# Kernel tuning notes

Hardware: AMD Instinct MI355X
Metric: run time of the kernel (lower is better)

## Reference

```python
import jax, jax.numpy as jnp
import numpy as np

N = 8192       # n_nodes
D = 256        # conf.unify['dim']
GAMMA = 3.0    # conf.unify['gamma']
ALPHA = 0.5    # conf.unify['alpha']
EPS = 1e-6


def setup_inputs() -> dict:
    key = jax.random.key(0)
    k1, k2, k3, k4 = jax.random.split(key, 4)
    z = jax.random.normal(k1, (N, D), dtype=jnp.float32)
    # kaiming-uniform-ish scale for W
    W = jax.random.normal(k2, (D, D), dtype=jnp.float32) * (1.0 / np.sqrt(D))
    beta = jax.random.uniform(k3, (N, 1), dtype=jnp.float32)      # beta_vector, init ~0.5
    Q = jax.random.uniform(k4, (N, N), dtype=jnp.float32)          # nonnegative prior (dense stand-in for sparse Q)
    return {"z": z, "W": W, "beta": beta, "Q": Q}


def reference(z, W, beta, Q):
    # init-time: Q row-normalized (normalize(Q, style='row'))
    Qn = Q / jnp.sum(Q, axis=1, keepdims=True)            # [N, N]

    # 1. similarity: sim = (z @ W) @ z.T
    sim = (z @ W) @ z.T                                    # [N, N]

    # 2. sparsify: relu(sim - beta), relu + eps, power 1/(gamma-1)
    adj = jax.nn.relu(sim - beta)                          # beta [N,1] broadcasts over columns
    adj = jax.nn.relu(adj) + EPS                           # relu_with_eps
    adj = adj ** (1.0 / (GAMMA - 1.0))                     # gamma power-law sparsify

    # 3. fuse Q: (1-alpha)*adj + alpha*(adj*Q), then /N
    adj = (1.0 - ALPHA) * adj + ALPHA * (adj * Qn)
    adj = adj / N

    # 4. row-normalize
    adj = adj / jnp.sum(adj, axis=-1, keepdims=True)
    return adj
```

## Files before the change

kernel.cpp:

```cpp
#include <hip/hip_runtime.h>
#include <hip/hip_bf16.h>
#include <math.h>

#define N 8192
#define D 256
#define EPSF 1e-6f

typedef __attribute__((ext_vector_type(8))) short short8v;
typedef __attribute__((ext_vector_type(4))) float f32x4;
typedef __attribute__((ext_vector_type(4))) unsigned short u16x4;

__device__ __forceinline__ unsigned short f2bf(float x) {
    __hip_bfloat16 h = __float2bfloat16(x);
    return *(unsigned short*)&h;
}
__device__ __forceinline__ float bf2f(unsigned short u) {
    __hip_bfloat16 h = *(__hip_bfloat16*)&u;
    return __bfloat162float(h);
}
__device__ __forceinline__ float bfu2f(unsigned short u) {
    unsigned int x = ((unsigned int)u) << 16;
    float f;
    __builtin_memcpy(&f, &x, 4);
    return f;
}
__device__ __forceinline__ f32x4 ntload4(const float* p) {
    return __builtin_nontemporal_load((const f32x4*)p);
}
__device__ __forceinline__ void ntstore4(float* p, f32x4 v) {
    __builtin_nontemporal_store(v, (f32x4*)p);
}

#define GLOAD_LDS16(gp, lp)                                                                  \
    __builtin_amdgcn_global_load_lds((const __attribute__((address_space(1))) unsigned int*)(gp), \
                                     (__attribute__((address_space(3))) unsigned int*)(lp), 16, 0, 0)

__global__ __launch_bounds__(256) void split_kernel(const float* __restrict__ x,
                                                    unsigned short* __restrict__ hi,
                                                    unsigned short* __restrict__ lo) {
    int i = (blockIdx.x * 256 + threadIdx.x) * 4;
    float4 v = *(const float4*)&x[i];
    ushort4 h, l;
    float a;
    a = v.x; h.x = f2bf(a); l.x = f2bf(a - bf2f(h.x));
    a = v.y; h.y = f2bf(a); l.y = f2bf(a - bf2f(h.y));
    a = v.z; h.z = f2bf(a); l.z = f2bf(a - bf2f(h.z));
    a = v.w; h.w = f2bf(a); l.w = f2bf(a - bf2f(h.w));
    *(ushort4*)&hi[i] = h;
    *(ushort4*)&lo[i] = l;
}

__global__ __launch_bounds__(256) void zw_kernel(const float* __restrict__ z,
                                                 const float* __restrict__ W,
                                                 unsigned short* __restrict__ Ah,
                                                 unsigned short* __restrict__ Al) {
    __shared__ float zs[32 * D];
    int rowBase = blockIdx.x * 32;
    const float4* zg = (const float4*)(z + (size_t)rowBase * D);
    float4* zs4 = (float4*)zs;
    for (int i = threadIdx.x; i < 32 * D / 4; i += 256) zs4[i] = zg[i];
    __syncthreads();

    float acc[32];
#pragma unroll
    for (int r = 0; r < 32; ++r) acc[r] = 0.f;
    int col = threadIdx.x;
    for (int kb = 0; kb < D; kb += 4) {
        float w0 = W[(size_t)(kb + 0) * D + col];
        float w1 = W[(size_t)(kb + 1) * D + col];
        float w2 = W[(size_t)(kb + 2) * D + col];
        float w3 = W[(size_t)(kb + 3) * D + col];
#pragma unroll
        for (int r = 0; r < 32; ++r) {
            float4 zv = *(const float4*)&zs[r * D + kb];
            acc[r] = fmaf(zv.x, w0, acc[r]);
            acc[r] = fmaf(zv.y, w1, acc[r]);
            acc[r] = fmaf(zv.z, w2, acc[r]);
            acc[r] = fmaf(zv.w, w3, acc[r]);
        }
    }
#pragma unroll
    for (int r = 0; r < 32; ++r) {
        float a = acc[r];
        unsigned short h = f2bf(a);
        unsigned short l = f2bf(a - bf2f(h));
        Ah[(size_t)(rowBase + r) * D + col] = h;
        Al[(size_t)(rowBase + r) * D + col] = l;
    }
}

__device__ __forceinline__ void tile_map(int bid, int& rowBase, int& colBase) {
    int xcd = bid & 7;
    int idx = bid >> 3;
    int bx = idx >> 3;
    int by = xcd * 8 + (idx & 7);
    rowBase = by * 128;
    colBase = bx * 128;
}

template <bool BF16S>
__global__ __launch_bounds__(256, 4) void gemm_s_kernel(
    const unsigned short* __restrict__ Ah, const unsigned short* __restrict__ Al,
    const unsigned short* __restrict__ Bh, const unsigned short* __restrict__ Bl,
    const float* __restrict__ beta, unsigned short* __restrict__ sbf,
    float* __restrict__ sf32) {
    __shared__ unsigned short lds[4][128][32];

    int rowBase, colBase;
    tile_map(blockIdx.x, rowBase, colBase);

    int t = threadIdx.x;
    int lane = t & 63;
    int w = t >> 6;
    int wr = w >> 1, wc = w & 1;
    int fr = lane & 15;
    int fg = lane >> 4;

    const unsigned short* tsrc = (w == 0) ? Ah : (w == 1) ? Al : (w == 2) ? Bh : Bl;
    int tRB = (w < 2) ? rowBase : colBase;
    int slot_src = (lane & 3) ^ ((lane >> 3) & 3);
    const unsigned short* gt = tsrc + (size_t)(tRB + (lane >> 2)) * D + slot_src * 8;

    f32x4 acc[4][4];
#pragma unroll
    for (int m = 0; m < 4; ++m)
#pragma unroll
        for (int n = 0; n < 4; ++n) acc[m][n] = (f32x4){0.f, 0.f, 0.f, 0.f};

    for (int kt = 0; kt < D; kt += 32) {
        __syncthreads();
#pragma unroll
        for (int j = 0; j < 8; ++j) {
            GLOAD_LDS16(gt + kt + j * 16 * D, &lds[w][j * 16][0]);
        }
        __syncthreads();

        short8v bhf[4], blf[4];
#pragma unroll
        for (int n = 0; n < 4; ++n) {
            int row = wc * 64 + n * 16 + fr;
            int sl = fg ^ ((row >> 1) & 3);
            bhf[n] = *(const short8v*)&lds[2][row][sl * 8];
            blf[n] = *(const short8v*)&lds[3][row][sl * 8];
        }
#pragma unroll
        for (int m = 0; m < 4; ++m) {
            int row = wr * 64 + m * 16 + fr;
            int sl = fg ^ ((row >> 1) & 3);
            short8v ahf = *(const short8v*)&lds[0][row][sl * 8];
            short8v alf = *(const short8v*)&lds[1][row][sl * 8];
#pragma unroll
            for (int n = 0; n < 4; ++n) {
                acc[m][n] = __builtin_amdgcn_mfma_f32_16x16x32_bf16(ahf, bhf[n], acc[m][n], 0, 0, 0);
                acc[m][n] = __builtin_amdgcn_mfma_f32_16x16x32_bf16(ahf, blf[n], acc[m][n], 0, 0, 0);
                acc[m][n] = __builtin_amdgcn_mfma_f32_16x16x32_bf16(alf, bhf[n], acc[m][n], 0, 0, 0);
            }
        }
    }

    __syncthreads();
    float* scratch = (float*)lds + w * (16 * 68);

#pragma unroll
    for (int m = 0; m < 4; ++m) {
#pragma unroll
        for (int n = 0; n < 4; ++n)
#pragma unroll
            for (int reg = 0; reg < 4; ++reg)
                scratch[(fg * 4 + reg) * 68 + n * 16 + fr] = acc[m][n][reg];

#pragma unroll
        for (int sub = 0; sub < 4; ++sub) {
            int rloc = sub * 4 + fg;
            int i = rowBase + wr * 64 + m * 16 + rloc;
            int col = colBase + wc * 64 + fr * 4;
            float4 sv = *(const float4*)&scratch[rloc * 68 + fr * 4];
            float bi = beta[i];
            float s0 = sqrtf(fmaxf(sv.x - bi, 0.f) + EPSF);
            float s1 = sqrtf(fmaxf(sv.y - bi, 0.f) + EPSF);
            float s2 = sqrtf(fmaxf(sv.z - bi, 0.f) + EPSF);
            float s3 = sqrtf(fmaxf(sv.w - bi, 0.f) + EPSF);
            if constexpr (BF16S) {
                u16x4 o = {f2bf(s0), f2bf(s1), f2bf(s2), f2bf(s3)};
                __builtin_nontemporal_store(o, (u16x4*)(sbf + (size_t)i * N + col));
            } else {
                f32x4 o = {s0, s1, s2, s3};
                ntstore4(sf32 + (size_t)i * N + col, o);
            }
        }
        __syncthreads();
    }
}

template <bool BF16S>
__global__ __launch_bounds__(512) void rownorm_kernel(float* __restrict__ out,
                                                      const float* __restrict__ Q,
                                                      const unsigned short* __restrict__ sbf) {
    __shared__ short8v sb[N / 8];
    __shared__ short8v qb[N / 8];
    __shared__ float red[24];

    int row = blockIdx.x;
    int t = threadIdx.x;
    const float* qrow = Q + (size_t)row * N;

    float ps = 0.f, pq = 0.f, qs = 0.f;
    for (int k = t; k < N / 8; k += 512) {
        float s[8];
        short8v spack;
        if constexpr (BF16S) {
            spack = __builtin_nontemporal_load((const short8v*)(sbf + (size_t)row * N + k * 8));
#pragma unroll
            for (int j = 0; j < 8; ++j) s[j] = bfu2f((unsigned short)spack[j]);
        } else {
            f32x4 a = ntload4(out + (size_t)row * N + k * 8);
            f32x4 b = ntload4(out + (size_t)row * N + k * 8 + 4);
            s[0] = a.x; s[1] = a.y; s[2] = a.z; s[3] = a.w;
            s[4] = b.x; s[5] = b.y; s[6] = b.z; s[7] = b.w;
#pragma unroll
            for (int j = 0; j < 8; ++j) spack[j] = (short)f2bf(s[j]);
        }
        sb[k] = spack;
        f32x4 q0 = ntload4(qrow + k * 8);
        f32x4 q1 = ntload4(qrow + k * 8 + 4);
        float q[8] = {q0.x, q0.y, q0.z, q0.w, q1.x, q1.y, q1.z, q1.w};
        short8v qpack;
#pragma unroll
        for (int j = 0; j < 8; ++j) qpack[j] = (short)f2bf(q[j]);
        qb[k] = qpack;
#pragma unroll
        for (int j = 0; j < 8; ++j) {
            ps += s[j];
            pq += s[j] * q[j];
            qs += q[j];
        }
    }
#pragma unroll
    for (int off = 1; off < 64; off <<= 1) {
        ps += __shfl_xor(ps, off, 64);
        pq += __shfl_xor(pq, off, 64);
        qs += __shfl_xor(qs, off, 64);
    }
    if ((t & 63) == 0) {
        int wv = t >> 6;
        red[wv * 3 + 0] = ps;
        red[wv * 3 + 1] = pq;
        red[wv * 3 + 2] = qs;
    }
    __syncthreads();
    float tps = 0.f, tpq = 0.f, tqs = 0.f;
#pragma unroll
    for (int i = 0; i < 8; ++i) {
        tps += red[i * 3 + 0];
        tpq += red[i * 3 + 1];
        tqs += red[i * 3 + 2];
    }
    float sh = 0.5f / tqs;
    float wv = 1.0f / (0.5f * tps + sh * tpq);

    float* orow = out + (size_t)row * N;
    for (int k = t; k < N / 8; k += 512) {
        short8v sp = sb[k];
        short8v qp = qb[k];
        f32x4 o0, o1;
#pragma unroll
        for (int j = 0; j < 4; ++j)
            o0[j] = bfu2f((unsigned short)sp[j]) * fmaf(bfu2f((unsigned short)qp[j]), sh, 0.5f) * wv;
#pragma unroll
        for (int j = 0; j < 4; ++j)
            o1[j] = bfu2f((unsigned short)sp[j + 4]) * fmaf(bfu2f((unsigned short)qp[j + 4]), sh, 0.5f) * wv;
        ntstore4(orow + k * 8, o0);
        ntstore4(orow + k * 8 + 4, o1);
    }
}

extern "C" void kernel_launch(void* const* d_in, const int* in_sizes, int n_in,
                              void* d_out, int out_size, void* d_ws, size_t ws_size,
                              hipStream_t stream) {
    const float* z = (const float*)d_in[0];
    const float* W = (const float*)d_in[1];
    const float* beta = (const float*)d_in[2];
    const float* Q = (const float*)d_in[3];
    float* out = (float*)d_out;

    unsigned short* Ah = (unsigned short*)d_ws;
    unsigned short* Al = Ah + (size_t)N * D;
    unsigned short* Bh = Al + (size_t)N * D;
    unsigned short* Bl = Bh + (size_t)N * D;
    unsigned short* sbf = Bl + (size_t)N * D;

    size_t need = 4 * (size_t)N * D * sizeof(unsigned short) + (size_t)N * N * sizeof(unsigned short);
    bool bf16s = (ws_size >= need);

    split_kernel<<<(N * D / 4) / 256, 256, 0, stream>>>(z, Bh, Bl);
    zw_kernel<<<N / 32, 256, 0, stream>>>(z, W, Ah, Al);
    if (bf16s) {
        gemm_s_kernel<true><<<4096, 256, 0, stream>>>(Ah, Al, Bh, Bl, beta, sbf, nullptr);
        rownorm_kernel<true><<<N, 512, 0, stream>>>(out, Q, sbf);
    } else {
        gemm_s_kernel<false><<<4096, 256, 0, stream>>>(Ah, Al, Bh, Bl, beta, nullptr, out);
        rownorm_kernel<false><<<N, 512, 0, stream>>>(out, Q, nullptr);
    }
}
```

Measured before the change: 303.7 us.

## Enlarge similarity GEMM tile to 256x256 with double-buffered LDS prefetch

The similarity GEMM moves from 128x128 tiles with 256 threads to 256x256 tiles with 512 threads, so each block reuses its A and B operands across four times as much output. The K loop now double-buffers LDS: the next K slice is staged while the current one feeds the MFMAs, which cuts one barrier per iteration. MFMA sections are wrapped in s_setprio. The trade-off is 128KB of LDS per block, which limits the kernel to one block per CU and leaves fewer blocks to hide latency. Correctness also depends on the async global-to-LDS loads having completed before the single per-iteration barrier.

```diff
diff --git a/kernel.cpp b/kernel.cpp
--- a/kernel.cpp
+++ b/kernel.cpp
@@ -89,80 +89,88 @@
     }
 }
 
-__device__ __forceinline__ void tile_map(int bid, int& rowBase, int& colBase) {
-    int xcd = bid & 7;
-    int idx = bid >> 3;
-    int bx = idx >> 3;
-    int by = xcd * 8 + (idx & 7);
-    rowBase = by * 128;
-    colBase = bx * 128;
-}
-
 template <bool BF16S>
-__global__ __launch_bounds__(256, 4) void gemm_s_kernel(
+__global__ __launch_bounds__(512, 2) void gemm_s_kernel(
     const unsigned short* __restrict__ Ah, const unsigned short* __restrict__ Al,
     const unsigned short* __restrict__ Bh, const unsigned short* __restrict__ Bl,
     const float* __restrict__ beta, unsigned short* __restrict__ sbf,
     float* __restrict__ sf32) {
-    __shared__ unsigned short lds[4][128][32];
-
-    int rowBase, colBase;
-    tile_map(blockIdx.x, rowBase, colBase);
+    __shared__ unsigned short lds[2][4][256][32];
+
+    int bid = blockIdx.x;
+    int xcd = bid & 7;
+    int idx = bid >> 3;
+    int rowIn = idx & 3;
+    int bx = idx >> 2;
+    int by = xcd * 4 + rowIn;
+    int rowBase = by * 256;
+    int colBase = bx * 256;
 
     int t = threadIdx.x;
     int lane = t & 63;
     int w = t >> 6;
-    int wr = w >> 1, wc = w & 1;
+    int wr = w >> 2, wc = w & 3;
     int fr = lane & 15;
     int fg = lane >> 4;
 
-    const unsigned short* tsrc = (w == 0) ? Ah : (w == 1) ? Al : (w == 2) ? Bh : Bl;
-    int tRB = (w < 2) ? rowBase : colBase;
+    int mat = w & 3;
+    int half = w >> 2;
+    const unsigned short* tsrc = (mat == 0) ? Ah : (mat == 1) ? Al : (mat == 2) ? Bh : Bl;
+    int tRB = (mat < 2) ? rowBase : colBase;
     int slot_src = (lane & 3) ^ ((lane >> 3) & 3);
-    const unsigned short* gt = tsrc + (size_t)(tRB + (lane >> 2)) * D + slot_src * 8;
-
-    f32x4 acc[4][4];
-#pragma unroll
-    for (int m = 0; m < 4; ++m)
+    const unsigned short* gt =
+        tsrc + (size_t)(tRB + half * 128 + (lane >> 2)) * D + slot_src * 8;
+
+    f32x4 acc[8][4];
+#pragma unroll
+    for (int m = 0; m < 8; ++m)
 #pragma unroll
         for (int n = 0; n < 4; ++n) acc[m][n] = (f32x4){0.f, 0.f, 0.f, 0.f};
 
+    auto stage = [&](int buf, int kt) {
+#pragma unroll
+        for (int j = 0; j < 8; ++j)
+            GLOAD_LDS16(gt + kt + j * 16 * D, &lds[buf][mat][half * 128 + j * 16][0]);
+    };
+
+    stage(0, 0);
+    int cur = 0;
     for (int kt = 0; kt < D; kt += 32) {
         __syncthreads();
-#pragma unroll
-        for (int j = 0; j < 8; ++j) {
-            GLOAD_LDS16(gt + kt + j * 16 * D, &lds[w][j * 16][0]);
-        }
-        __syncthreads();
-
-        short8v bhf[4], blf[4];
+        if (kt + 32 < D) stage(cur ^ 1, kt + 32);
+        __builtin_amdgcn_sched_barrier(0);
+
+        short8v bh[4], bl[4];
 #pragma unroll
         for (int n = 0; n < 4; ++n) {
             int row = wc * 64 + n * 16 + fr;
-            int sl = fg ^ ((row >> 1) & 3);
-            bhf[n] = *(const short8v*)&lds[2][row][sl * 8];
-            blf[n] = *(const short8v*)&lds[3][row][sl * 8];
-        }
-#pragma unroll
-        for (int m = 0; m < 4; ++m) {
-            int row = wr * 64 + m * 16 + fr;
-            int sl = fg ^ ((row >> 1) & 3);
-            short8v ahf = *(const short8v*)&lds[0][row][sl * 8];
-            short8v alf = *(const short8v*)&lds[1][row][sl * 8];
+            int sl = fg ^ ((fr >> 1) & 3);
+            bh[n] = *(const short8v*)&lds[cur][2][row][sl * 8];
+            bl[n] = *(const short8v*)&lds[cur][3][row][sl * 8];
+        }
+        __builtin_amdgcn_s_setprio(1);
+#pragma unroll
+        for (int m = 0; m < 8; ++m) {
+            int row = wr * 128 + m * 16 + fr;
+            int sl = fg ^ ((fr >> 1) & 3);
+            short8v ah = *(const short8v*)&lds[cur][0][row][sl * 8];
+            short8v al = *(const short8v*)&lds[cur][1][row][sl * 8];
 #pragma unroll
             for (int n = 0; n < 4; ++n) {
-                acc[m][n] = __builtin_amdgcn_mfma_f32_16x16x32_bf16(ahf, bhf[n], acc[m][n], 0, 0, 0);
-                acc[m][n] = __builtin_amdgcn_mfma_f32_16x16x32_bf16(ahf, blf[n], acc[m][n], 0, 0, 0);
-                acc[m][n] = __builtin_amdgcn_mfma_f32_16x16x32_bf16(alf, bhf[n], acc[m][n], 0, 0, 0);
+                acc[m][n] = __builtin_amdgcn_mfma_f32_16x16x32_bf16(ah, bh[n], acc[m][n], 0, 0, 0);
+                acc[m][n] = __builtin_amdgcn_mfma_f32_16x16x32_bf16(ah, bl[n], acc[m][n], 0, 0, 0);
+                acc[m][n] = __builtin_amdgcn_mfma_f32_16x16x32_bf16(al, bh[n], acc[m][n], 0, 0, 0);
             }
         }
+        __builtin_amdgcn_s_setprio(0);
+        cur ^= 1;
     }
 
     __syncthreads();
     float* scratch = (float*)lds + w * (16 * 68);
 
 #pragma unroll
-    for (int m = 0; m < 4; ++m) {
+    for (int m = 0; m < 8; ++m) {
 #pragma unroll
         for (int n = 0; n < 4; ++n)
 #pragma unroll
@@ -172,7 +180,7 @@
 #pragma unroll
         for (int sub = 0; sub < 4; ++sub) {
             int rloc = sub * 4 + fg;
-            int i = rowBase + wr * 64 + m * 16 + rloc;
+            int i = rowBase + wr * 128 + m * 16 + rloc;
             int col = colBase + wc * 64 + fr * 4;
             float4 sv = *(const float4*)&scratch[rloc * 68 + fr * 4];
             float bi = beta[i];
@@ -295,10 +303,10 @@
     split_kernel<<<(N * D / 4) / 256, 256, 0, stream>>>(z, Bh, Bl);
     zw_kernel<<<N / 32, 256, 0, stream>>>(z, W, Ah, Al);
     if (bf16s) {
-        gemm_s_kernel<true><<<4096, 256, 0, stream>>>(Ah, Al, Bh, Bl, beta, sbf, nullptr);
+        gemm_s_kernel<true><<<1024, 512, 0, stream>>>(Ah, Al, Bh, Bl, beta, sbf, nullptr);
         rownorm_kernel<true><<<N, 512, 0, stream>>>(out, Q, sbf);
     } else {
-        gemm_s_kernel<false><<<4096, 256, 0, stream>>>(Ah, Al, Bh, Bl, beta, nullptr, out);
+        gemm_s_kernel<false><<<1024, 512, 0, stream>>>(Ah, Al, Bh, Bl, beta, nullptr, out);
         rownorm_kernel<false><<<N, 512, 0, stream>>>(out, Q, nullptr);
     }
 }
```

Result: no change. 303.7 us (-0.0%).
